# Optimization experiments

Hardware: AMD Instinct MI355X
Metric: run time of the kernel (lower is better)

The kernel has to match this reference:

```python
import jax, jax.numpy as jnp
import numpy as np
from jax import lax

B, H, W = 32, 30, 30          # batch of ARC-style grids (max 30x30)
D, NH = 256, 4                # hidden_dim, num_heads (ARPSConfig)
L, P = 8, 12                  # max_program_length, number of primitives
NUM_COLORS = 10
PAINT_COLOR = 3


def setup_inputs() -> dict:
    key = jax.random.key(0)
    ks = jax.random.split(key, 11)
    s = 0.02
    return {
        "grid": jax.random.randint(ks[0], (B, H, W), 0, NUM_COLORS, dtype=jnp.int32),
        "anchor": jax.random.randint(ks[1], (B, 2), 0, min(H, W), dtype=jnp.int32),
        "embed": jax.random.normal(ks[2], (NUM_COLORS, D), jnp.float32) * s,
        "pos_emb": jax.random.normal(ks[3], (H * W, D), jnp.float32) * s,
        "wq": jax.random.normal(ks[4], (D, D), jnp.float32) * s,
        "wk": jax.random.normal(ks[5], (D, D), jnp.float32) * s,
        "wv": jax.random.normal(ks[6], (D, D), jnp.float32) * s,
        "wo": jax.random.normal(ks[7], (D, D), jnp.float32) * s,
        "step_q": jax.random.normal(ks[8], (L, D), jnp.float32) * s,
        "w_out": jax.random.normal(ks[9], (D, P), jnp.float32) * s,
        "b_out": jnp.zeros((P,), jnp.float32),
    }


def _mha(q, k, v, nh):
    b, lq, d = q.shape
    hd = d // nh
    qh = q.reshape(b, lq, nh, hd)
    kh = k.reshape(b, k.shape[1], nh, hd)
    vh = v.reshape(b, v.shape[1], nh, hd)
    scores = jnp.einsum('bqhd,bkhd->bhqk', qh, kh) / jnp.sqrt(jnp.asarray(hd, q.dtype))
    attn = jax.nn.softmax(scores, axis=-1)
    return jnp.einsum('bhqk,bkhd->bqhd', attn, vh).reshape(b, lq, d)


def _execute_one(grid, anchor):
    """Fixed anchor-relative program: select_connected((0,0)) -> rotate_90 -> paint."""
    h, w = grid.shape
    ar = jnp.clip(anchor[0], 0, h - 1)
    ac = jnp.clip(anchor[1], 0, w - 1)
    # --- select_connected: 4-connected component of seed color (parallel flood fill) ---
    seed_color = grid[ar, ac]
    same = grid == seed_color
    m0 = jnp.zeros((h, w), bool).at[ar, ac].set(True)

    def dilate(m):
        p = jnp.pad(m, 1)
        return m | p[:-2, 1:-1] | p[2:, 1:-1] | p[1:-1, :-2] | p[1:-1, 2:]

    def body(st):
        m = st[0]
        nm = dilate(m) & same
        return (nm, jnp.any(nm != m))

    mask, _ = lax.while_loop(lambda st: st[1], body, (m0, jnp.array(True)))
    sel = mask.astype(jnp.float32)
    # --- rotate_90 clockwise around anchor: (dr,dc) -> (dc,-dr); out-of-bounds dropped ---
    rr = jnp.broadcast_to(jnp.arange(h)[:, None], (h, w))
    cc = jnp.broadcast_to(jnp.arange(w)[None, :], (h, w))
    nr = ar + (cc - ac)
    nc = ac - (rr - ar)
    rot = jnp.zeros_like(sel).at[nr, nc].set(sel, mode='drop')
    # --- paint: overwrite selected pixels with PAINT_COLOR ---
    return jnp.where(rot > 0.5, jnp.int32(PAINT_COLOR), grid)


def reference(grid, anchor, embed, pos_emb, wq, wk, wv, wo, step_q, w_out, b_out):
    b = grid.shape[0]
    tok = embed[grid.reshape(b, -1)] + pos_emb                  # (B, T=900, D)
    tok = tok + _mha(tok @ wq, tok @ wk, tok @ wv, NH) @ wo     # self-attn over pixels
    sq = jnp.broadcast_to(step_q, (b,) + step_q.shape)          # (B, L, D) step queries
    hsteps = _mha(sq @ wq, tok @ wk, tok @ wv, NH) @ wo         # cross-attn: steps -> pixels
    logits = hsteps @ w_out + b_out                             # (B, L, P) primitive logits
    out_grid = jax.vmap(_execute_one)(grid, anchor)             # (B, H, W) executed program
    return logits, out_grid
```

## Files before the change

kernel.cpp:

```cpp
#include <hip/hip_runtime.h>


typedef __attribute__((ext_vector_type(8))) short bf16x8;
typedef __attribute__((ext_vector_type(4))) float f32x4;

__device__ __forceinline__ short f2bf(float f) {
  union { float f; unsigned u; } v; v.f = f;
  unsigned r = v.u + 0x7fffu + ((v.u >> 16) & 1u);
  return (short)(r >> 16);
}
__device__ __forceinline__ float bf2f(short s) {
  union { unsigned u; float f; } v; v.u = ((unsigned)(unsigned short)s) << 16;
  return v.f;
}
__device__ __forceinline__ unsigned cvt_pk_bf16(float lo, float hi) {
  unsigned r;
  asm("v_cvt_pk_bf16_f32 %0, %1, %2" : "=v"(r) : "v"(lo), "v"(hi));
  return r;
}
__device__ __forceinline__ int swz(int row, int col) {
  return row * 64 + ((((col >> 3) ^ row) & 7) << 3) + (col & 7);
}
__device__ __forceinline__ int a256(int row, int col) {
  return row * 256 + (col & ~63) + (((((col >> 3) & 7) ^ row) & 7) << 3);
}
__device__ __forceinline__ void gload16(const short* gsrc, short* lds) {
  __builtin_amdgcn_global_load_lds(
      (const __attribute__((address_space(1))) unsigned int*)gsrc,
      (__attribute__((address_space(3))) unsigned int*)lds, 16, 0, 0);
}

constexpr size_t OFF_POSQ  = 0;
constexpr size_t OFF_POSK  = 230400;
constexpr size_t OFF_POSV  = 460800;
constexpr size_t OFF_EMBQ  = 691200;
constexpr size_t OFF_EMBK  = 693760;
constexpr size_t OFF_EMBV  = 696320;
constexpr size_t OFF_WOOUT = 698880;
constexpr size_t OFF_Q2    = 701952;
constexpr size_t OFF_QP    = 704000;
constexpr size_t OFF_QE    = OFF_QP + 28800;
constexpr size_t OFF_WVO   = OFF_QE + 512;
constexpr size_t OFF_Q2K   = OFF_WVO + 12288;
constexpr size_t OFF_F32_END = 769536;
constexpr size_t SOFF_WOKVT = 0;
constexpr size_t SOFF_ATTN  = 131072;
constexpr size_t SOFF_KB    = 7503872;
constexpr size_t SOFF_VT    = 14876672;
constexpr size_t SOFF_E     = SOFF_KB;
constexpr size_t SOFF_UPART = SOFF_KB + 983040;
constexpr size_t SOFF_VPART = SOFF_UPART + 2097152;

__global__ void k_small(const float* __restrict__ embed,
                        const float* __restrict__ wq,
                        const float* __restrict__ wk,
                        const float* __restrict__ wv,
                        const float* __restrict__ wo,
                        const float* __restrict__ step_q,
                        const float* __restrict__ w_out,
                        float* __restrict__ ws) {
  const int blk = blockIdx.x;
  int job, base;
  if      (blk < 10)  { job = 0; base = blk; }
  else if (blk < 20)  { job = 1; base = blk - 10; }
  else if (blk < 30)  { job = 2; base = blk - 20; }
  else if (blk < 42)  { job = 3; base = blk - 30; }
  else                { job = 4; base = blk - 42; }
  const float* A; const float* Wm; float* C; int M; int N;
  switch (job) {
    case 0: A=embed;  Wm=wq;    C=ws+OFF_EMBQ;  M=10;  N=256; break;
    case 1: A=embed;  Wm=wk;    C=ws+OFF_EMBK;  M=10;  N=256; break;
    case 2: A=embed;  Wm=wv;    C=ws+OFF_EMBV;  M=10;  N=256; break;
    case 3: A=wo;     Wm=w_out; C=ws+OFF_WOOUT; M=256; N=12;  break;
    default:A=step_q; Wm=wq;    C=ws+OFF_Q2;    M=8;   N=256; break;
  }
  int idx = base * 256 + threadIdx.x;
  if (idx >= M * N) return;
  int m = idx / N, n = idx - m * N;
  const float* a = A + (size_t)m * 256;
  float acc = 0.f;
  #pragma unroll 8
  for (int k = 0; k < 256; ++k) acc = fmaf(a[k], Wm[(size_t)k * N + n], acc);
  C[idx] = acc;
}

__global__ __launch_bounds__(256) void k_gemm_all(const float* __restrict__ pos_emb,
                                                  const float* __restrict__ wq,
                                                  const float* __restrict__ wk,
                                                  const float* __restrict__ wv,
                                                  const float* __restrict__ wo,
                                                  float* __restrict__ ws) {
  const int mt = blockIdx.x, nt = blockIdx.y;
  const bool wojob = nt >= 12;
  if (wojob && mt >= 4) return;
  const float* A = wojob ? wo : pos_emb;
  const float* W;
  float* C = nullptr;
  int n0;
  int base_n = 0;
  if (!wojob) {
    W = nt < 4 ? wq : (nt < 8 ? wk : wv);
    C = ws + (nt < 4 ? OFF_POSQ : (nt < 8 ? OFF_POSK : OFF_POSV));
    n0 = (nt & 3) * 64;
  } else {
    W = nt < 16 ? wk : wv;
    base_n = nt < 16 ? 0 : 256;
    n0 = (nt & 3) * 64;
  }
  const int m0 = mt * 64;
  const int tid = threadIdx.x, tr = tid >> 4, tc = tid & 15;
  __shared__ float As[64][68];
  __shared__ float Bs[64][68];
  float acc[4][4] = {};
  for (int kc = 0; kc < 4; ++kc) {
    __syncthreads();
    for (int i = tid; i < 1024; i += 256) {
      int row = i >> 4, c4 = (i & 15) * 4;
      int m = m0 + row; if (m > 899) m = 899;
      *(float4*)&As[row][c4] = *(const float4*)&A[(size_t)m * 256 + kc * 64 + c4];
      *(float4*)&Bs[row][c4] = *(const float4*)&W[(size_t)(kc * 64 + row) * 256 + n0 + c4];
    }
    __syncthreads();
    #pragma unroll 8
    for (int kk = 0; kk < 64; ++kk) {
      float a0 = As[4*tr+0][kk], a1 = As[4*tr+1][kk];
      float a2 = As[4*tr+2][kk], a3 = As[4*tr+3][kk];
      float4 b4 = *(const float4*)&Bs[kk][4*tc];
      acc[0][0]+=a0*b4.x; acc[0][1]+=a0*b4.y; acc[0][2]+=a0*b4.z; acc[0][3]+=a0*b4.w;
      acc[1][0]+=a1*b4.x; acc[1][1]+=a1*b4.y; acc[1][2]+=a1*b4.z; acc[1][3]+=a1*b4.w;
      acc[2][0]+=a2*b4.x; acc[2][1]+=a2*b4.y; acc[2][2]+=a2*b4.z; acc[2][3]+=a2*b4.w;
      acc[3][0]+=a3*b4.x; acc[3][1]+=a3*b4.y; acc[3][2]+=a3*b4.z; acc[3][3]+=a3*b4.w;
    }
  }
  if (!wojob) {
    #pragma unroll
    for (int i = 0; i < 4; ++i) {
      int m = m0 + 4 * tr + i;
      if (m < 900)
        *(float4*)&C[(size_t)m * 256 + n0 + 4 * tc] =
            make_float4(acc[i][0], acc[i][1], acc[i][2], acc[i][3]);
    }
  } else {
    __syncthreads();
    #pragma unroll
    for (int i = 0; i < 4; ++i)
      #pragma unroll
      for (int j = 0; j < 4; ++j)
        Bs[4 * tc + j][4 * tr + i] = acc[i][j];
    __syncthreads();
    short* wokvT = (short*)(ws + OFF_F32_END) + SOFF_WOKVT;
    for (int i = tid; i < 512; i += 256) {
      int row = i >> 3, ch = i & 7;
      union { short s[8]; bf16x8 v; } u;
      #pragma unroll
      for (int jj = 0; jj < 8; ++jj) u.s[jj] = f2bf(Bs[row][ch * 8 + jj]);
      *(bf16x8*)&wokvT[(size_t)(base_n + n0 + row) * 256 + m0 + ch * 8] = u.v;
    }
  }
}

__global__ __launch_bounds__(256) void k_pre2(float* __restrict__ ws) {
  const float* q2 = ws + OFF_Q2;
  const short* wokvT = (const short*)(ws + OFF_F32_END) + SOFF_WOKVT;
  const int blk = blockIdx.x, tid = threadIdx.x;
  if (blk < 32) {
    int lh = blk, h = lh >> 3, l = lh & 7;
    __shared__ float qs[64];
    if (tid < 64) qs[tid] = q2[l * 256 + h * 64 + tid];
    __syncthreads();
    float acc = 0.f;
    for (int dd = 0; dd < 64; ++dd)
      acc = fmaf(qs[dd], bf2f(wokvT[(size_t)(h * 64 + dd) * 256 + tid]), acc);
    ((short*)(ws + OFF_Q2K))[lh * 256 + tid] = f2bf(acc);
  } else if (blk < 64) {
    int lh = blk - 32, h = lh >> 3, l = lh & 7;
    __shared__ float qs[64];
    if (tid < 64) qs[tid] = q2[l * 256 + h * 64 + tid];
    __syncthreads();
    const float* posK = ws + OFF_POSK;
    for (int t = tid; t < 900; t += 256) {
      float acc = 0.f;
      const float* pr = posK + (size_t)t * 256 + h * 64;
      #pragma unroll 8
      for (int dd = 0; dd < 64; ++dd) acc = fmaf(qs[dd], pr[dd], acc);
      ws[OFF_QP + (size_t)lh * 900 + t] = acc;
    }
  } else if (blk == 64) {
    const float* embK = ws + OFF_EMBK;
    if (tid < 320) {
      int lh = tid / 10, c = tid - lh * 10;
      int h = lh >> 3, l = lh & 7;
      float acc = 0.f;
      const float* qrow = q2 + l * 256 + h * 64;
      const float* er = embK + (size_t)c * 256 + h * 64;
      for (int dd = 0; dd < 64; ++dd) acc = fmaf(qrow[dd], er[dd], acc);
      ws[OFF_QE + lh * 16 + c] = acc;
    }
  } else {
    int h = blk - 65;
    const float* woOut = ws + OFF_WOOUT;
    __shared__ float wos[64][12];
    for (int i = tid; i < 768; i += 256) wos[i / 12][i % 12] = woOut[(h * 64 + i / 12) * 12 + i % 12];
    __syncthreads();
    float acc[12] = {};
    for (int dd = 0; dd < 64; ++dd) {
      float v = bf2f(wokvT[(size_t)(256 + h * 64 + dd) * 256 + tid]);
      #pragma unroll
      for (int p = 0; p < 12; ++p) acc[p] = fmaf(v, wos[dd][p], acc[p]);
    }
    #pragma unroll
    for (int p = 0; p < 12; ++p)
      ws[OFF_WVO + ((size_t)h * 256 + tid) * 12 + p] = acc[p];
  }
}

__global__ __launch_bounds__(256) void k_kv(const int* __restrict__ grid_in,
                                            const float* __restrict__ ws,
                                            short* __restrict__ Kb,
                                            short* __restrict__ VT) {
  const int kt = blockIdx.x, b = blockIdx.y;
  const int t0 = kt * 64, tid = threadIdx.x;
  const float* posK = ws + OFF_POSK;
  const float* embK = ws + OFF_EMBK;
  const float* posV = ws + OFF_POSV;
  const float* embV = ws + OFF_EMBV;

  for (int i = tid; i < 2048; i += 256) {
    int row = i >> 5, ch = i & 31;
    int t = t0 + row;
    if (t > 899) continue;
    int g = grid_in[b * 900 + t];
    const float* pk = posK + (size_t)t * 256 + ch * 8;
    const float* ek = embK + (size_t)g * 256 + ch * 8;
    float4 p0 = *(const float4*)pk, p1 = *(const float4*)(pk + 4);
    float4 e0 = *(const float4*)ek, e1 = *(const float4*)(ek + 4);
    union { short s[8]; bf16x8 v; } u;
    u.s[0] = f2bf(p0.x + e0.x); u.s[1] = f2bf(p0.y + e0.y);
    u.s[2] = f2bf(p0.z + e0.z); u.s[3] = f2bf(p0.w + e0.w);
    u.s[4] = f2bf(p1.x + e1.x); u.s[5] = f2bf(p1.y + e1.y);
    u.s[6] = f2bf(p1.z + e1.z); u.s[7] = f2bf(p1.w + e1.w);
    *(bf16x8*)&Kb[((size_t)(b * 900 + t)) * 256 + ch * 8] = u.v;
  }

  __shared__ float Lf[64 * 65];
  const int tt = tid & 63, dq = tid >> 6;
  for (int h = 0; h < 4; ++h) {
    __syncthreads();
    for (int i = tid; i < 512; i += 256) {
      int row = i >> 3, ch = i & 7;
      int t = t0 + row; if (t > 899) t = 899;
      int g = grid_in[b * 900 + t];
      const float* pv = posV + (size_t)t * 256 + h * 64 + ch * 8;
      const float* ev = embV + (size_t)g * 256 + h * 64 + ch * 8;
      float4 p0 = *(const float4*)pv, p1 = *(const float4*)(pv + 4);
      float4 e0 = *(const float4*)ev, e1 = *(const float4*)(ev + 4);
      float* L = &Lf[row * 65 + ch * 8];
      L[0] = p0.x + e0.x; L[1] = p0.y + e0.y; L[2] = p0.z + e0.z; L[3] = p0.w + e0.w;
      L[4] = p1.x + e1.x; L[5] = p1.y + e1.y; L[6] = p1.z + e1.z; L[7] = p1.w + e1.w;
    }
    __syncthreads();
    short* tile = VT + ((size_t)((b * 4 + h) * 15 + kt)) * 4096;
    #pragma unroll
    for (int dd = 0; dd < 16; ++dd) {
      int d = dq * 16 + dd;
      tile[d * 64 + tt] = f2bf(Lf[tt * 65 + d]);
    }
  }
}

__global__ __launch_bounds__(256) void k_attn(const int* __restrict__ grid_in,
                                              const float* __restrict__ ws,
                                              const short* __restrict__ Kb,
                                              const short* __restrict__ VT,
                                              short* __restrict__ attnOut) {
  const int bidx = blockIdx.x;
  const int bh = ((bidx >> 6) << 3) | (bidx & 7);
  const int qt = (bidx >> 3) & 7;
  const int h = bh & 3, b = bh >> 2;
  const int t0 = qt * 128, hc = h * 64;
  const int tid = threadIdx.x, w = tid >> 6, lane = tid & 63;
  const int g = lane >> 4, c16 = lane & 15;
  const size_t tileBase = (size_t)(bh * 15) * 4096;

  __shared__ __align__(16) short Ks[2][4096];
  __shared__ __align__(16) short Vs[2][4096];
  __shared__ __align__(16) short Ps[4096];

  const float* posQ = ws + OFF_POSQ;
  const float* embQ = ws + OFF_EMBQ;

  bf16x8 aQ[2][2];
  #pragma unroll
  for (int s = 0; s < 2; ++s) {
    int t = t0 + s * 64 + w * 16 + c16; if (t > 899) t = 899;
    int gq = grid_in[b * 900 + t];
    #pragma unroll
    for (int kc = 0; kc < 2; ++kc) {
      union { short s8[8]; bf16x8 v; } u;
      #pragma unroll
      for (int j = 0; j < 8; ++j) {
        int d = hc + kc * 32 + g * 8 + j;
        u.s8[j] = f2bf(0.125f * (embQ[gq * 256 + d] + posQ[(size_t)t * 256 + d]));
      }
      aQ[s][kc] = u.v;
    }
  }

#define STAGE(BUF, KT)                                                        \
  do {                                                                        \
    int kk0_ = (KT) * 64;                                                     \
    _Pragma("unroll")                                                         \
    for (int j_ = 0; j_ < 2; ++j_) {                                          \
      int c_ = j_ * 256 + w * 64 + lane;                                      \
      int row_ = c_ >> 3, ch_ = c_ & 7;                                       \
      int t_ = kk0_ + row_; if (t_ > 899) t_ = 899;                           \
      int sw_ = ((ch_ ^ row_) & 7) << 3;                                      \
      gload16(Kb + ((size_t)(b * 900 + t_)) * 256 + hc + sw_,                 \
              &Ks[BUF][(j_ * 256 + w * 64) << 3]);                            \
      gload16(VT + tileBase + (size_t)(KT) * 4096 + (row_ << 6) + sw_,        \
              &Vs[BUF][(j_ * 256 + w * 64) << 3]);                            \
    }                                                                         \
  } while (0)

  float l_[2] = {0.f, 0.f};
  f32x4 O[2][4];
  #pragma unroll
  for (int s = 0; s < 2; ++s)
    #pragma unroll
    for (int dt = 0; dt < 4; ++dt) { f32x4 z = {0.f,0.f,0.f,0.f}; O[s][dt] = z; }

  STAGE(0, 0);
  __syncthreads();

  int cur = 0;
  for (int kt = 0; kt < 15; ++kt) {
    if (kt + 1 < 15) STAGE(cur ^ 1, kt + 1);

    if (kt < 14) {
      f32x4 sacc[2][4];
      #pragma unroll
      for (int ct = 0; ct < 4; ++ct) {
        bf16x8 aK0 = *(bf16x8*)&Ks[cur][swz(ct * 16 + c16, g * 8)];
        bf16x8 aK1 = *(bf16x8*)&Ks[cur][swz(ct * 16 + c16, 32 + g * 8)];
        #pragma unroll
        for (int s = 0; s < 2; ++s) {
          f32x4 z = {0.f, 0.f, 0.f, 0.f};
          z = __builtin_amdgcn_mfma_f32_16x16x32_bf16(aK0, aQ[s][0], z, 0, 0, 0);
          z = __builtin_amdgcn_mfma_f32_16x16x32_bf16(aK1, aQ[s][1], z, 0, 0, 0);
          sacc[s][ct] = z;
        }
      }
      #pragma unroll
      for (int s = 0; s < 2; ++s) {
        float rs = 0.f;
        unsigned pk[4][2];
        #pragma unroll
        for (int ct = 0; ct < 4; ++ct) {
          float p0 = __expf(sacc[s][ct][0]);
          float p1 = __expf(sacc[s][ct][1]);
          float p2 = __expf(sacc[s][ct][2]);
          float p3 = __expf(sacc[s][ct][3]);
          rs += (p0 + p1) + (p2 + p3);
          pk[ct][0] = cvt_pk_bf16(p0, p1);
          pk[ct][1] = cvt_pk_bf16(p2, p3);
        }
        rs += __shfl_xor(rs, 16);
        rs += __shfl_xor(rs, 32);
        l_[s] += rs;
        #pragma unroll
        for (int ct = 0; ct < 4; ++ct)
          *(uint2*)&Ps[swz(w * 16 + c16, ct * 16 + 4 * g)] =
              make_uint2(pk[ct][0], pk[ct][1]);
        #pragma unroll
        for (int c = 0; c < 2; ++c) {
          bf16x8 aP = *(bf16x8*)&Ps[swz(w * 16 + c16, c * 32 + g * 8)];
          #pragma unroll
          for (int dt = 0; dt < 4; ++dt) {
            bf16x8 bV = *(bf16x8*)&Vs[cur][swz(dt * 16 + c16, c * 32 + g * 8)];
            O[s][dt] = __builtin_amdgcn_mfma_f32_16x16x32_bf16(aP, bV, O[s][dt], 0, 0, 0);
          }
        }
      }
    } else {
      bf16x8 aK0 = *(bf16x8*)&Ks[cur][swz(c16, g * 8)];
      bf16x8 aK1 = *(bf16x8*)&Ks[cur][swz(c16, 32 + g * 8)];
      #pragma unroll
      for (int s = 0; s < 2; ++s) {
        f32x4 z = {0.f, 0.f, 0.f, 0.f};
        z = __builtin_amdgcn_mfma_f32_16x16x32_bf16(aK0, aQ[s][0], z, 0, 0, 0);
        z = __builtin_amdgcn_mfma_f32_16x16x32_bf16(aK1, aQ[s][1], z, 0, 0, 0);
        float p0 = 0.f, p1 = 0.f, p2 = 0.f, p3 = 0.f;
        if (g == 0) {
          p0 = __expf(z[0]); p1 = __expf(z[1]);
          p2 = __expf(z[2]); p3 = __expf(z[3]);
        }
        float rs = (p0 + p1) + (p2 + p3);
        rs += __shfl_xor(rs, 16);
        rs += __shfl_xor(rs, 32);
        l_[s] += rs;
        *(uint2*)&Ps[swz(w * 16 + c16, 4 * g)] =
            make_uint2(cvt_pk_bf16(p0, p1), cvt_pk_bf16(p2, p3));
        *(uint2*)&Ps[swz(w * 16 + c16, 16 + 4 * g)] = make_uint2(0u, 0u);
        bf16x8 aP = *(bf16x8*)&Ps[swz(w * 16 + c16, g * 8)];
        #pragma unroll
        for (int dt = 0; dt < 4; ++dt) {
          bf16x8 bV = *(bf16x8*)&Vs[cur][swz(dt * 16 + c16, g * 8)];
          O[s][dt] = __builtin_amdgcn_mfma_f32_16x16x32_bf16(aP, bV, O[s][dt], 0, 0, 0);
        }
      }
    }

    __syncthreads();
    cur ^= 1;
  }
#undef STAGE

  #pragma unroll
  for (int s = 0; s < 2; ++s) {
    #pragma unroll
    for (int r = 0; r < 4; ++r) {
      float lq = __shfl(l_[s], (g << 4) | (4 * g + r));
      int t = t0 + s * 64 + w * 16 + 4 * g + r;
      if (t < 900) {
        float inv = 1.f / lq;
        #pragma unroll
        for (int dt = 0; dt < 4; ++dt)
          attnOut[((size_t)(b * 900 + t)) * 256 + hc + dt * 16 + c16] =
              f2bf(O[s][dt][r] * inv);
      }
    }
  }
}

__global__ __launch_bounds__(256) void k_crossA(const int* __restrict__ grid_in,
                                                const float* __restrict__ ws,
                                                const short* __restrict__ attnOut,
                                                short* __restrict__ E,
                                                float* __restrict__ Sp) {
  const int kt = blockIdx.x, b = blockIdx.y;
  const int t0 = kt * 64;
  const int tid = threadIdx.x, w = tid >> 6, lane = tid & 63;
  const int g = lane >> 4, c16 = lane & 15;
  __shared__ __align__(16) short Aat[16384];
  __shared__ __align__(16) short Qk[8192];
  __shared__ float qpL[32 * 72];
  __shared__ float qeL[512];
  __shared__ int   gtl[64];
  __shared__ float spW[128];

  #pragma unroll
  for (int it = 0; it < 8; ++it) {
    int idx = it * 256 + w * 64 + lane;
    int row = idx >> 5, ch = idx & 31;
    int t = t0 + row; if (t > 899) t = 899;
    int sw = (((ch & 7) ^ row) & 7) << 3;
    gload16(attnOut + ((size_t)(b * 900 + t)) * 256 + (ch >> 3) * 64 + sw,
            &Aat[(it * 256 + w * 64) << 3]);
  }
  const short* q2k = (const short*)(ws + OFF_Q2K);
  #pragma unroll
  for (int it = 0; it < 4; ++it) {
    int idx = it * 256 + w * 64 + lane;
    int row = idx >> 5, ch = idx & 31;
    int sw = (((ch & 7) ^ row) & 7) << 3;
    gload16(q2k + (size_t)row * 256 + (ch >> 3) * 64 + sw,
            &Qk[(it * 256 + w * 64) << 3]);
  }
  #pragma unroll
  for (int it = 0; it < 2; ++it) {
    int idx = it * 256 + tid, row = idx >> 4, c4 = (idx & 15) * 4;
    *(float4*)&qpL[row * 72 + c4] = *(const float4*)&ws[OFF_QP + (size_t)row * 900 + t0 + c4];
  }
  for (int idx = tid; idx < 512; idx += 256) qeL[idx] = ws[OFF_QE + idx];
  if (tid < 64) { int t = t0 + tid; gtl[tid] = grid_in[b * 900 + (t > 899 ? 899 : t)]; }
  __syncthreads();

  f32x4 sacc[2];
  { f32x4 z = {0.f,0.f,0.f,0.f}; sacc[0] = z; sacc[1] = z; }
  #pragma unroll
  for (int kk = 0; kk < 8; ++kk) {
    bf16x8 aA = *(bf16x8*)&Aat[a256(w * 16 + c16, kk * 32 + g * 8)];
    bf16x8 b0 = *(bf16x8*)&Qk[a256(c16, kk * 32 + g * 8)];
    bf16x8 b1 = *(bf16x8*)&Qk[a256(16 + c16, kk * 32 + g * 8)];
    sacc[0] = __builtin_amdgcn_mfma_f32_16x16x32_bf16(aA, b0, sacc[0], 0, 0, 0);
    sacc[1] = __builtin_amdgcn_mfma_f32_16x16x32_bf16(aA, b1, sacc[1], 0, 0, 0);
  }
  #pragma unroll
  for (int ct = 0; ct < 2; ++ct) {
    int lh = ct * 16 + c16;
    float e[4]; float rs = 0.f;
    #pragma unroll
    for (int r = 0; r < 4; ++r) {
      int tl = w * 16 + g * 4 + r;
      float s = 0.125f * (sacc[ct][r] + qpL[lh * 72 + tl] + qeL[lh * 16 + gtl[tl]]);
      e[r] = (t0 + tl < 900) ? __expf(s) : 0.f;
      rs += e[r];
    }
    *(uint2*)&E[((size_t)(b * 32 + lh)) * 960 + t0 + w * 16 + g * 4] =
        make_uint2(cvt_pk_bf16(e[0], e[1]), cvt_pk_bf16(e[2], e[3]));
    rs += __shfl_xor(rs, 16);
    rs += __shfl_xor(rs, 32);
    if (g == 0) spW[w * 32 + lh] = rs;
  }
  __syncthreads();
  if (tid < 32)
    Sp[((size_t)b * 32 + tid) * 15 + kt] =
        spW[tid] + spW[32 + tid] + spW[64 + tid] + spW[96 + tid];
}

__global__ __launch_bounds__(256) void k_crossP(const short* __restrict__ attnOut,
                                                const short* __restrict__ E,
                                                const short* __restrict__ VT,
                                                short* __restrict__ Upart,
                                                short* __restrict__ Vpart) {
  const int ktg = blockIdx.x, b = blockIdx.y;
  const int tid = threadIdx.x, w = tid >> 6, lane = tid & 63;
  const int g = lane >> 4, c16 = lane & 15;
  const int h = w, ctv = h >> 1;
  __shared__ __align__(16) short AT[256 * 72];
  __shared__ __align__(16) short Et[2048];
  __shared__ __align__(16) short VTl[16384];

  f32x4 Uacc[2][4], Vacc[4];
  { f32x4 z = {0.f,0.f,0.f,0.f};
    #pragma unroll
    for (int a = 0; a < 2; ++a)
      #pragma unroll
      for (int q = 0; q < 4; ++q) Uacc[a][q] = z;
    #pragma unroll
    for (int a = 0; a < 4; ++a) Vacc[a] = z; }

  const int ntile = (ktg < 7) ? 2 : 1;
  for (int tt = 0; tt < ntile; ++tt) {
    const int kt = ktg * 2 + tt, t0 = kt * 64;
    if (tt) __syncthreads();
    #pragma unroll
    for (int it = 0; it < 8; ++it) {
      int idx = it * 256 + tid;
      int tl = idx >> 5, jc = idx & 31;
      int t = t0 + tl; if (t > 899) t = 899;
      bf16x8 v = *(const bf16x8*)&attnOut[((size_t)(b * 900 + t)) * 256 + jc * 8];
      #pragma unroll
      for (int ii = 0; ii < 8; ++ii)
        AT[(jc * 8 + ii) * 72 + ((((tl >> 3) ^ jc) & 7) << 3) + (tl & 7)] = v[ii];
    }
    {
      int idx = w * 64 + lane;
      int row = idx >> 3, ch = idx & 7;
      int sw = ((ch ^ row) & 7) << 3;
      gload16(E + ((size_t)(b * 32 + row)) * 960 + t0 + sw, &Et[(w * 64) << 3]);
    }
    #pragma unroll
    for (int it = 0; it < 8; ++it) {
      int idx = it * 256 + w * 64 + lane;
      int hh = idx >> 9, rem = idx & 511;
      int row = rem >> 3, ch = rem & 7;
      int sw = ((ch ^ row) & 7) << 3;
      gload16(VT + ((size_t)((b * 4 + hh) * 15 + kt)) * 4096 + row * 64 + sw,
              &VTl[(it * 256 + w * 64) << 3]);
    }
    __syncthreads();
    #pragma unroll
    for (int kk = 0; kk < 2; ++kk) {
      bf16x8 aE0 = *(bf16x8*)&Et[swz(c16, kk * 32 + g * 8)];
      bf16x8 aE1 = *(bf16x8*)&Et[swz(16 + c16, kk * 32 + g * 8)];
      #pragma unroll
      for (int q = 0; q < 4; ++q) {
        int j = (w * 4 + q) * 16 + c16;
        int tch = kk * 4 + g;
        bf16x8 bA = *(bf16x8*)&AT[j * 72 + (((tch ^ (j >> 3)) & 7) << 3)];
        Uacc[0][q] = __builtin_amdgcn_mfma_f32_16x16x32_bf16(aE0, bA, Uacc[0][q], 0, 0, 0);
        Uacc[1][q] = __builtin_amdgcn_mfma_f32_16x16x32_bf16(aE1, bA, Uacc[1][q], 0, 0, 0);
      }
      bf16x8 bE = (ctv == 0) ? aE0 : aE1;
      #pragma unroll
      for (int rt = 0; rt < 4; ++rt) {
        bf16x8 aV = *(bf16x8*)&VTl[h * 4096 + swz(rt * 16 + c16, kk * 32 + g * 8)];
        Vacc[rt] = __builtin_amdgcn_mfma_f32_16x16x32_bf16(aV, bE, Vacc[rt], 0, 0, 0);
      }
    }
  }
  #pragma unroll
  for (int rt = 0; rt < 2; ++rt)
    #pragma unroll
    for (int q = 0; q < 4; ++q) {
      int j = (w * 4 + q) * 16 + c16;
      #pragma unroll
      for (int r = 0; r < 4; ++r) {
        int lh = rt * 16 + g * 4 + r;
        Upart[(((size_t)(ktg * 32 + b)) * 32 + lh) * 256 + j] = f2bf(Uacc[rt][q][r]);
      }
    }
  if ((c16 >> 3) == (h & 1)) {
    int l = c16 & 7;
    #pragma unroll
    for (int rt = 0; rt < 4; ++rt)
      #pragma unroll
      for (int r = 0; r < 4; ++r) {
        int d = rt * 16 + g * 4 + r;
        Vpart[((((size_t)(ktg * 32 + b)) * 4 + h) * 64 + d) * 8 + l] = f2bf(Vacc[rt][r]);
      }
  }
}

__global__ void k_crossR(const float* __restrict__ ws,
                         const float* __restrict__ b_out,
                         const short* __restrict__ Upart,
                         const short* __restrict__ Vpart,
                         const float* __restrict__ Sp,
                         float* __restrict__ out) {
  const int bl = blockIdx.x, b = bl >> 3, l = bl & 7;
  const int tid = threadIdx.x;
  __shared__ float Us[4][256];
  __shared__ float Vsm[4][64];
  __shared__ float Sinv[4];
  __shared__ float part[4][12];
  for (int h = 0; h < 4; ++h) {
    int lh = h * 8 + l;
    for (int j = tid; j < 256; j += 64) {
      float a = 0.f;
      #pragma unroll
      for (int kg = 0; kg < 8; ++kg)
        a += bf2f(Upart[(((size_t)(kg * 32 + b)) * 32 + lh) * 256 + j]);
      Us[h][j] = a;
    }
    float a = 0.f;
    #pragma unroll
    for (int kg = 0; kg < 8; ++kg)
      a += bf2f(Vpart[((((size_t)(kg * 32 + b)) * 4 + h) * 64 + tid) * 8 + l]);
    Vsm[h][tid] = a;
  }
  if (tid < 4) {
    int lh = tid * 8 + l;
    float s = 0.f;
    #pragma unroll
    for (int k = 0; k < 15; ++k) s += Sp[((size_t)b * 32 + lh) * 15 + k];
    Sinv[tid] = 1.f / s;
  }
  __syncthreads();
  if (tid < 48) {
    int h = tid / 12, p = tid % 12;
    const float* woOut = ws + OFF_WOOUT;
    const float* WVO = ws + OFF_WVO;
    float acc = 0.f;
    for (int dd = 0; dd < 64; ++dd)
      acc = fmaf(Vsm[h][dd], woOut[(h * 64 + dd) * 12 + p], acc);
    for (int j = 0; j < 256; ++j)
      acc = fmaf(Us[h][j], WVO[((size_t)h * 256 + j) * 12 + p], acc);
    part[h][p] = acc * Sinv[h];
  }
  __syncthreads();
  if (tid < 12)
    out[(size_t)bl * 12 + tid] =
        b_out[tid] + part[0][tid] + part[1][tid] + part[2][tid] + part[3][tid];
}

__global__ void k_execute(const int* __restrict__ grid_in,
                          const int* __restrict__ anchor,
                          float* __restrict__ outg) {
  const int b = blockIdx.x;
  const int lane = threadIdx.x;
  const int* g = grid_in + b * 900;
  int ar = anchor[2 * b], ac = anchor[2 * b + 1];
  ar = min(max(ar, 0), 29); ac = min(max(ac, 0), 29);
  const int seed = g[ar * 30 + ac];

  unsigned same = 0u;
  if (lane < 30)
    for (int c = 0; c < 30; ++c) same |= (unsigned)(g[lane * 30 + c] == seed) << c;

  unsigned cur = (lane == ar) ? (1u << ac) : 0u;
  bool changed = true;
  while (changed) {
    unsigned up = __shfl(cur, (lane + 63) & 63);
    unsigned dn = __shfl(cur, (lane + 1) & 63);
    if (lane == 0) up = 0u;
    unsigned nm = (cur | (cur << 1) | (cur >> 1) | up | dn) & same;
    changed = __any(nm != cur);
    cur = nm;
  }

  __shared__ unsigned msh[32];
  if (lane < 32) msh[lane] = (lane < 30) ? cur : 0u;
  __syncthreads();

  if (lane < 30) {
    unsigned rot = 0u;
    int cc = lane - ar + ac;
    if (cc >= 0 && cc < 30) {
      for (int nc = 0; nc < 30; ++nc) {
        int rr = ar + ac - nc;
        if (rr >= 0 && rr < 30) rot |= ((msh[rr] >> cc) & 1u) << nc;
      }
    }
    for (int c = 0; c < 30; ++c) {
      int v = ((rot >> c) & 1u) ? 3 : g[lane * 30 + c];
      outg[b * 900 + lane * 30 + c] = (float)v;
    }
  }
}

extern "C" void kernel_launch(void* const* d_in, const int* in_sizes, int n_in,
                              void* d_out, int out_size, void* d_ws, size_t ws_size,
                              hipStream_t stream) {
  const int*   grid_in = (const int*)d_in[0];
  const int*   anchor  = (const int*)d_in[1];
  const float* embed   = (const float*)d_in[2];
  const float* pos_emb = (const float*)d_in[3];
  const float* wq      = (const float*)d_in[4];
  const float* wk      = (const float*)d_in[5];
  const float* wv      = (const float*)d_in[6];
  const float* wo      = (const float*)d_in[7];
  const float* step_q  = (const float*)d_in[8];
  const float* w_out   = (const float*)d_in[9];
  const float* b_out   = (const float*)d_in[10];
  float* out = (float*)d_out;
  float* ws  = (float*)d_ws;
  short* wsS = (short*)(ws + OFF_F32_END);

  k_small<<<dim3(50), dim3(256), 0, stream>>>(embed, wq, wk, wv, wo, step_q, w_out, ws);
  k_gemm_all<<<dim3(15, 20), dim3(256), 0, stream>>>(pos_emb, wq, wk, wv, wo, ws);
  k_pre2<<<dim3(69), dim3(256), 0, stream>>>(ws);
  k_kv<<<dim3(15, 32), dim3(256), 0, stream>>>(grid_in, ws,
                                               wsS + SOFF_KB, wsS + SOFF_VT);
  k_attn<<<dim3(1024), dim3(256), 0, stream>>>(grid_in, ws, wsS + SOFF_KB,
                                               wsS + SOFF_VT, wsS + SOFF_ATTN);
  short* E  = wsS + SOFF_E;
  float* Sp = (float*)(wsS + SOFF_WOKVT);
  k_crossA<<<dim3(15, 32), dim3(256), 0, stream>>>(grid_in, ws, wsS + SOFF_ATTN, E, Sp);
  k_crossP<<<dim3(8, 32), dim3(256), 0, stream>>>(wsS + SOFF_ATTN, E, wsS + SOFF_VT,
                                                  wsS + SOFF_UPART, wsS + SOFF_VPART);
  k_crossR<<<dim3(256), dim3(64), 0, stream>>>(ws, b_out, wsS + SOFF_UPART,
                                               wsS + SOFF_VPART, Sp, out);
  k_execute<<<dim3(32), dim3(64), 0, stream>>>(grid_in, anchor, out + 32 * 8 * 12);
}
```

Baseline: 245.1 us.

## Merge small-GEMM and projection kernels, vectorize VT stores, use exp2 softmax

Folds k_small and k_gemm_all into one k_pre launch over a flat 262-block grid, saving a launch and dropping the blocks the old 2D grid wasted on early return. The V-transpose store in k_kv now packs eight bf16 values into one 16-byte write instead of scattered 2-byte stores. Softmax scaling switches to 0.125*log2(e) with the hardware exp2 builtin, removing the multiply hidden inside __expf. Whether the scaled score also feeds paths that expect natural-log scaling needs checking elsewhere.

```diff
diff --git a/kernel.cpp b/kernel.cpp
--- a/kernel.cpp
+++ b/kernel.cpp
@@ -3,6 +3,8 @@
 
 typedef __attribute__((ext_vector_type(8))) short bf16x8;
 typedef __attribute__((ext_vector_type(4))) float f32x4;
+
+constexpr float kScl = 0.18033688011112042f;
 
 __device__ __forceinline__ short f2bf(float f) {
   union { float f; unsigned u; } v; v.f = f;
@@ -17,6 +19,9 @@
   unsigned r;
   asm("v_cvt_pk_bf16_f32 %0, %1, %2" : "=v"(r) : "v"(lo), "v"(hi));
   return r;
+}
+__device__ __forceinline__ float exp2f_fast(float x) {
+  return __builtin_amdgcn_exp2f(x);
 }
 __device__ __forceinline__ int swz(int row, int col) {
   return row * 64 + ((((col >> 3) ^ row) & 7) << 3) + (col & 7);
@@ -51,64 +56,61 @@
 constexpr size_t SOFF_UPART = SOFF_KB + 983040;
 constexpr size_t SOFF_VPART = SOFF_UPART + 2097152;
 
-__global__ void k_small(const float* __restrict__ embed,
-                        const float* __restrict__ wq,
-                        const float* __restrict__ wk,
-                        const float* __restrict__ wv,
-                        const float* __restrict__ wo,
-                        const float* __restrict__ step_q,
-                        const float* __restrict__ w_out,
-                        float* __restrict__ ws) {
+__global__ __launch_bounds__(256) void k_pre(const float* __restrict__ pos_emb,
+                                             const float* __restrict__ embed,
+                                             const float* __restrict__ wq,
+                                             const float* __restrict__ wk,
+                                             const float* __restrict__ wv,
+                                             const float* __restrict__ wo,
+                                             const float* __restrict__ step_q,
+                                             const float* __restrict__ w_out,
+                                             float* __restrict__ ws) {
   const int blk = blockIdx.x;
-  int job, base;
-  if      (blk < 10)  { job = 0; base = blk; }
-  else if (blk < 20)  { job = 1; base = blk - 10; }
-  else if (blk < 30)  { job = 2; base = blk - 20; }
-  else if (blk < 42)  { job = 3; base = blk - 30; }
-  else                { job = 4; base = blk - 42; }
-  const float* A; const float* Wm; float* C; int M; int N;
-  switch (job) {
-    case 0: A=embed;  Wm=wq;    C=ws+OFF_EMBQ;  M=10;  N=256; break;
-    case 1: A=embed;  Wm=wk;    C=ws+OFF_EMBK;  M=10;  N=256; break;
-    case 2: A=embed;  Wm=wv;    C=ws+OFF_EMBV;  M=10;  N=256; break;
-    case 3: A=wo;     Wm=w_out; C=ws+OFF_WOOUT; M=256; N=12;  break;
-    default:A=step_q; Wm=wq;    C=ws+OFF_Q2;    M=8;   N=256; break;
-  }
-  int idx = base * 256 + threadIdx.x;
-  if (idx >= M * N) return;
-  int m = idx / N, n = idx - m * N;
-  const float* a = A + (size_t)m * 256;
-  float acc = 0.f;
-  #pragma unroll 8
-  for (int k = 0; k < 256; ++k) acc = fmaf(a[k], Wm[(size_t)k * N + n], acc);
-  C[idx] = acc;
-}
-
-__global__ __launch_bounds__(256) void k_gemm_all(const float* __restrict__ pos_emb,
-                                                  const float* __restrict__ wq,
-                                                  const float* __restrict__ wk,
-                                                  const float* __restrict__ wv,
-                                                  const float* __restrict__ wo,
-                                                  float* __restrict__ ws) {
-  const int mt = blockIdx.x, nt = blockIdx.y;
-  const bool wojob = nt >= 12;
-  if (wojob && mt >= 4) return;
-  const float* A = wojob ? wo : pos_emb;
-  const float* W;
-  float* C = nullptr;
-  int n0;
-  int base_n = 0;
-  if (!wojob) {
+  const int tid = threadIdx.x;
+  if (blk >= 212) {
+    const int b2 = blk - 212;
+    int job, base;
+    if      (b2 < 10) { job = 0; base = b2; }
+    else if (b2 < 20) { job = 1; base = b2 - 10; }
+    else if (b2 < 30) { job = 2; base = b2 - 20; }
+    else if (b2 < 42) { job = 3; base = b2 - 30; }
+    else              { job = 4; base = b2 - 42; }
+    const float* A; const float* Wm; float* C; int M; int N;
+    switch (job) {
+      case 0: A=embed;  Wm=wq;    C=ws+OFF_EMBQ;  M=10;  N=256; break;
+      case 1: A=embed;  Wm=wk;    C=ws+OFF_EMBK;  M=10;  N=256; break;
+      case 2: A=embed;  Wm=wv;    C=ws+OFF_EMBV;  M=10;  N=256; break;
+      case 3: A=wo;     Wm=w_out; C=ws+OFF_WOOUT; M=256; N=12;  break;
+      default:A=step_q; Wm=wq;    C=ws+OFF_Q2;    M=8;   N=256; break;
+    }
+    int idx = base * 256 + tid;
+    if (idx >= M * N) return;
+    int m = idx / N, n = idx - m * N;
+    const float* a = A + (size_t)m * 256;
+    float acc = 0.f;
+    #pragma unroll 8
+    for (int k = 0; k < 256; ++k) acc = fmaf(a[k], Wm[(size_t)k * N + n], acc);
+    C[idx] = acc;
+    return;
+  }
+
+  bool wojob; int mt, n0, base_n = 0;
+  const float* A; const float* W; float* C = nullptr;
+  if (blk < 180) {
+    wojob = false; mt = blk % 15; int nt = blk / 15;
+    A = pos_emb;
     W = nt < 4 ? wq : (nt < 8 ? wk : wv);
     C = ws + (nt < 4 ? OFF_POSQ : (nt < 8 ? OFF_POSK : OFF_POSV));
     n0 = (nt & 3) * 64;
   } else {
-    W = nt < 16 ? wk : wv;
-    base_n = nt < 16 ? 0 : 256;
-    n0 = (nt & 3) * 64;
+    wojob = true; int j = blk - 180; mt = j & 3; int nt2 = j >> 2;
+    A = wo;
+    W = nt2 < 4 ? wk : wv;
+    base_n = nt2 < 4 ? 0 : 256;
+    n0 = (nt2 & 3) * 64;
   }
   const int m0 = mt * 64;
-  const int tid = threadIdx.x, tr = tid >> 4, tc = tid & 15;
+  const int tr = tid >> 4, tc = tid & 15;
   __shared__ float As[64][68];
   __shared__ float Bs[64][68];
   float acc[4][4] = {};
@@ -243,7 +245,6 @@
   }
 
   __shared__ float Lf[64 * 65];
-  const int tt = tid & 63, dq = tid >> 6;
   for (int h = 0; h < 4; ++h) {
     __syncthreads();
     for (int i = tid; i < 512; i += 256) {
@@ -261,9 +262,14 @@
     __syncthreads();
     short* tile = VT + ((size_t)((b * 4 + h) * 15 + kt)) * 4096;
     #pragma unroll
-    for (int dd = 0; dd < 16; ++dd) {
-      int d = dq * 16 + dd;
-      tile[d * 64 + tt] = f2bf(Lf[tt * 65 + d]);
+    for (int u = 0; u < 2; ++u) {
+      int unit = u * 256 + tid;
+      int d = unit >> 3;
+      int t8 = (unit & 7) * 8;
+      union { short s[8]; bf16x8 v; } p;
+      #pragma unroll
+      for (int i = 0; i < 8; ++i) p.s[i] = f2bf(Lf[(t8 + i) * 65 + d]);
+      *(bf16x8*)&tile[d * 64 + t8] = p.v;
     }
   }
 }
@@ -300,7 +306,7 @@
       #pragma unroll
       for (int j = 0; j < 8; ++j) {
         int d = hc + kc * 32 + g * 8 + j;
-        u.s8[j] = f2bf(0.125f * (embQ[gq * 256 + d] + posQ[(size_t)t * 256 + d]));
+        u.s8[j] = f2bf(kScl * (embQ[gq * 256 + d] + posQ[(size_t)t * 256 + d]));
       }
       aQ[s][kc] = u.v;
     }
@@ -356,10 +362,10 @@
         unsigned pk[4][2];
         #pragma unroll
         for (int ct = 0; ct < 4; ++ct) {
-          float p0 = __expf(sacc[s][ct][0]);
-          float p1 = __expf(sacc[s][ct][1]);
-          float p2 = __expf(sacc[s][ct][2]);
-          float p3 = __expf(sacc[s][ct][3]);
+          float p0 = exp2f_fast(sacc[s][ct][0]);
+          float p1 = exp2f_fast(sacc[s][ct][1]);
+          float p2 = exp2f_fast(sacc[s][ct][2]);
+          float p3 = exp2f_fast(sacc[s][ct][3]);
           rs += (p0 + p1) + (p2 + p3);
           pk[ct][0] = cvt_pk_bf16(p0, p1);
           pk[ct][1] = cvt_pk_bf16(p2, p3);
@@ -391,8 +397,8 @@
         z = __builtin_amdgcn_mfma_f32_16x16x32_bf16(aK1, aQ[s][1], z, 0, 0, 0);
         float p0 = 0.f, p1 = 0.f, p2 = 0.f, p3 = 0.f;
         if (g == 0) {
-          p0 = __expf(z[0]); p1 = __expf(z[1]);
-          p2 = __expf(z[2]); p3 = __expf(z[3]);
+          p0 = exp2f_fast(z[0]); p1 = exp2f_fast(z[1]);
+          p2 = exp2f_fast(z[2]); p3 = exp2f_fast(z[3]);
         }
         float rs = (p0 + p1) + (p2 + p3);
         rs += __shfl_xor(rs, 16);
@@ -492,8 +498,8 @@
     #pragma unroll
     for (int r = 0; r < 4; ++r) {
       int tl = w * 16 + g * 4 + r;
-      float s = 0.125f * (sacc[ct][r] + qpL[lh * 72 + tl] + qeL[lh * 16 + gtl[tl]]);
-      e[r] = (t0 + tl < 900) ? __expf(s) : 0.f;
+      float s = kScl * (sacc[ct][r] + qpL[lh * 72 + tl] + qeL[lh * 16 + gtl[tl]]);
+      e[r] = (t0 + tl < 900) ? exp2f_fast(s) : 0.f;
       rs += e[r];
     }
     *(uint2*)&E[((size_t)(b * 32 + lh)) * 960 + t0 + w * 16 + g * 4] =
@@ -718,8 +724,8 @@
   float* ws  = (float*)d_ws;
   short* wsS = (short*)(ws + OFF_F32_END);
 
-  k_small<<<dim3(50), dim3(256), 0, stream>>>(embed, wq, wk, wv, wo, step_q, w_out, ws);
-  k_gemm_all<<<dim3(15, 20), dim3(256), 0, stream>>>(pos_emb, wq, wk, wv, wo, ws);
+  k_pre<<<dim3(262), dim3(256), 0, stream>>>(pos_emb, embed, wq, wk, wv, wo,
+                                             step_q, w_out, ws);
   k_pre2<<<dim3(69), dim3(256), 0, stream>>>(ws);
   k_kv<<<dim3(15, 32), dim3(256), 0, stream>>>(grid_in, ws,
                                                wsS + SOFF_KB, wsS + SOFF_VT);
```

New measurement: 226.6 us. 7.6% less time.
